# Performance work log

Measured on AMD Instinct MI355X. Metric: run time of the kernel, lower is better.

Reference implementation:

```python
import jax, jax.numpy as jnp
import numpy as np

D_MODEL = 1024
D_FF = 286
NUM_REL = 2
EPS = 1e-6


def setup_inputs() -> dict:
    key = jax.random.key(0)
    ks = jax.random.split(key, 8)
    N, E = 20000, 320000
    hidden_states = jax.random.normal(ks[0], (N, D_MODEL), dtype=jnp.float32)
    edge_index = jax.random.randint(ks[1], (2, E), 0, N, dtype=jnp.int64)
    edge_type = jax.random.randint(ks[2], (E,), 0, NUM_REL, dtype=jnp.int64)
    # learned parameters
    ln_weight = jnp.ones((D_MODEL,), dtype=jnp.float32)
    W_rel = jax.random.normal(ks[3], (NUM_REL, D_MODEL, D_FF), dtype=jnp.float32) * (1.0 / np.sqrt(D_MODEL))
    W_root = jax.random.normal(ks[4], (D_MODEL, D_FF), dtype=jnp.float32) * (1.0 / np.sqrt(D_MODEL))
    conv_bias = jnp.zeros((D_FF,), dtype=jnp.float32)
    wo_weight = jax.random.normal(ks[5], (D_FF, D_MODEL), dtype=jnp.float32) * (1.0 / np.sqrt(D_FF))
    return {"hidden_states": hidden_states, "edge_index": edge_index, "edge_type": edge_type,
            "ln_weight": ln_weight, "W_rel": W_rel, "W_root": W_root,
            "conv_bias": conv_bias, "wo_weight": wo_weight}


def t5_layer_norm(x, weight):
    # T5-style: RMS only, no mean subtraction, no bias; variance in fp32
    var = jnp.mean(jnp.square(x.astype(jnp.float32)), axis=-1, keepdims=True)
    return weight * (x * jax.lax.rsqrt(var + EPS))


def rgcn_conv(x, edge_index, edge_type, W_rel, W_root, bias):
    # PyG RGCNConv with aggr='mean' per relation, root weight, bias.
    N = x.shape[0]
    src, dst = edge_index[0], edge_index[1]
    h_src = x[src]  # [E, d_model] gather
    out = x @ W_root + bias  # root term, [N, d_ff]
    for r in range(NUM_REL):
        w = (edge_type == r).astype(x.dtype)  # [E]
        msg = (h_src @ W_rel[r]) * w[:, None]  # [E, d_ff]
        sums = jax.ops.segment_sum(msg, dst, num_segments=N)  # [N, d_ff]
        cnt = jax.ops.segment_sum(w, dst, num_segments=N)  # [N]
        out = out + sums / jnp.maximum(cnt, 1.0)[:, None]
    return out


def reference(hidden_states, edge_index, edge_type, ln_weight, W_rel, W_root, conv_bias, wo_weight):
    norm_x = t5_layer_norm(hidden_states, ln_weight)
    y = jax.nn.elu(rgcn_conv(norm_x, edge_index, edge_type, W_rel, W_root, conv_bias))
    # dropout layers are identity in eval mode
    y = y @ wo_weight  # [N, d_model], Linear(d_ff, d_model, bias=False)
    return hidden_states + y
```

## Files before the change

kernel.cpp:

```cpp
#include <hip/hip_runtime.h>
#include <hip/hip_bf16.h>


typedef __bf16  bf16x8  __attribute__((ext_vector_type(8)));
typedef float   floatx4 __attribute__((ext_vector_type(4)));

#define NNODE   20000
#define DMODEL  1024
#define DFF     286
#define DFFP    288
#define NDW     144
#define NPAIR   72

typedef __attribute__((address_space(1))) const void* gptr_t;
typedef __attribute__((address_space(3))) void*       lptr_t;

struct alignas(8) bf4 { __bf16 x, y, z, w; };

__device__ __forceinline__ float bflo(unsigned u) {
    union { unsigned u; float f; } c; c.u = u << 16; return c.f;
}
__device__ __forceinline__ float bfhi(unsigned u) {
    union { unsigned u; float f; } c; c.u = u & 0xffff0000u; return c.f;
}
__device__ __forceinline__ unsigned packbf(float a, float b) {
    union { __bf16 h[2]; unsigned u; } c;
    c.h[0] = (__bf16)a; c.h[1] = (__bf16)b; return c.u;
}
__device__ __forceinline__ float elu1(float v) {
    return v > 0.0f ? v : (expf(v) - 1.0f);
}

__global__ __launch_bounds__(256) void k_transpose_cast(
    const float* __restrict__ src, __bf16* __restrict__ dst,
    int K, int N, int Kout, int Nout)
{
    __shared__ float t[32][33];
    int tx = threadIdx.x & 31, ty = threadIdx.x >> 5;
    int k0 = blockIdx.x * 32, n0 = blockIdx.y * 32;
    #pragma unroll
    for (int r = 0; r < 4; ++r) {
        int k = k0 + ty + r * 8, n = n0 + tx;
        t[ty + r * 8][tx] = (k < K && n < N) ? src[(size_t)k * N + n] : 0.0f;
    }
    __syncthreads();
    #pragma unroll
    for (int r = 0; r < 4; ++r) {
        int n = n0 + ty + r * 8, k = k0 + tx;
        if (n < Nout && k < Kout) dst[(size_t)n * Kout + k] = (__bf16)t[tx][ty + r * 8];
    }
}

__global__ __launch_bounds__(256) void k_rmsnorm(
    const float* __restrict__ x, const float* __restrict__ w,
    __bf16* __restrict__ out)
{
    int row = blockIdx.x;
    int t = threadIdx.x;
    float4 v = reinterpret_cast<const float4*>(x + (size_t)row * DMODEL)[t];
    float ss = v.x * v.x + v.y * v.y + v.z * v.z + v.w * v.w;
    #pragma unroll
    for (int off = 32; off; off >>= 1) ss += __shfl_down(ss, off, 64);
    __shared__ float red[4];
    int lane = t & 63, wv = t >> 6;
    if (lane == 0) red[wv] = ss;
    __syncthreads();
    float tot = red[0] + red[1] + red[2] + red[3];
    float scale = rsqrtf(tot * (1.0f / (float)DMODEL) + 1e-6f);
    float4 wv4 = reinterpret_cast<const float4*>(w)[t];
    bf4 o;
    o.x = (__bf16)(v.x * scale * wv4.x);
    o.y = (__bf16)(v.y * scale * wv4.y);
    o.z = (__bf16)(v.z * scale * wv4.z);
    o.w = (__bf16)(v.w * scale * wv4.w);
    reinterpret_cast<bf4*>(out + (size_t)row * DMODEL)[t] = o;
}

__global__ __launch_bounds__(256, 2) void k_gemm1(
    const __bf16* __restrict__ A, const __bf16* __restrict__ Broot,
    const __bf16* __restrict__ Brel, __bf16* __restrict__ P)
{
    const int bid = blockIdx.x;
    const int mt = bid / 3, mz = bid - mt * 3;
    const __bf16* B = (mz == 0) ? Broot : (Brel + (size_t)(mz - 1) * DFFP * DMODEL);
    __bf16* out = P + (size_t)mz * NNODE * DFFP;

    const int m0 = mt * 128;
    const int tid = threadIdx.x;
    const int lane = tid & 63, wave = tid >> 6;
    const int wm = wave >> 1, wn = wave & 1;
    const int quad = lane >> 4, l16 = lane & 15;

    __shared__ __align__(16) __bf16 As[128 * 32];
    __shared__ __align__(16) __bf16 Bs[288 * 32];

    floatx4 zero = {0.f, 0.f, 0.f, 0.f};
    floatx4 acc[4][9];
    #pragma unroll
    for (int i = 0; i < 4; ++i)
        #pragma unroll
        for (int j = 0; j < 9; ++j) acc[i][j] = zero;

    const int crow = lane >> 2;
    const int ccol = (lane & 3) * 8;

    for (int k0 = 0; k0 < DMODEL; k0 += 32) {
        #pragma unroll
        for (int ii = 0; ii < 7; ++ii) {
            int c = wave + ii * 4;
            if (c < 8) {
                int row = c * 16 + crow;
                int grow = m0 + row; if (grow > NNODE - 1) grow = NNODE - 1;
                __builtin_amdgcn_global_load_lds(
                    (gptr_t)(A + (size_t)grow * DMODEL + k0 + ccol),
                    (lptr_t)(As + c * 512), 16, 0, 0);
            } else if (c < 26) {
                int nrow = (c - 8) * 16 + crow;
                __builtin_amdgcn_global_load_lds(
                    (gptr_t)(B + (size_t)nrow * DMODEL + k0 + ccol),
                    (lptr_t)(Bs + (c - 8) * 512), 16, 0, 0);
            }
        }
        __syncthreads();
        bf16x8 af[4], bq[9];
        #pragma unroll
        for (int i = 0; i < 4; ++i)
            af[i] = *reinterpret_cast<const bf16x8*>(As + (wm * 64 + i * 16 + l16) * 32 + quad * 8);
        #pragma unroll
        for (int j = 0; j < 9; ++j)
            bq[j] = *reinterpret_cast<const bf16x8*>(Bs + (wn * 144 + j * 16 + l16) * 32 + quad * 8);
        #pragma unroll
        for (int i = 0; i < 4; ++i)
            #pragma unroll
            for (int j = 0; j < 9; ++j)
                acc[i][j] = __builtin_amdgcn_mfma_f32_16x16x32_bf16(af[i], bq[j], acc[i][j], 0, 0, 0);
        __syncthreads();
    }
    #pragma unroll
    for (int i = 0; i < 4; ++i) {
        int rbase = m0 + wm * 64 + i * 16 + quad * 4;
        #pragma unroll
        for (int j = 0; j < 9; ++j) {
            int col = wn * 144 + j * 16 + l16;
            #pragma unroll
            for (int rr = 0; rr < 4; ++rr) {
                int row = rbase + rr;
                if (row < NNODE) out[(size_t)row * DFFP + col] = (__bf16)acc[i][j][rr];
            }
        }
    }
}

__global__ __launch_bounds__(256) void k_hist(
    const int* __restrict__ ei, int* __restrict__ bcnt, int E)
{
    int t = blockIdx.x * 256 + threadIdx.x;
    if (t < E) atomicAdd(&bcnt[ei[E + t]], 1);
}

__global__ __launch_bounds__(1024) void k_scan(
    const int* __restrict__ bcnt, int* __restrict__ boff, int* __restrict__ bcur)
{
    const int CH = 20;
    __shared__ int s[1024];
    int t = threadIdx.x;
    int base = t * CH;
    int loc[CH];
    int sum = 0;
    #pragma unroll
    for (int i = 0; i < CH; ++i) {
        int idx = base + i;
        int v = (idx < NNODE) ? bcnt[idx] : 0;
        loc[i] = sum; sum += v;
    }
    s[t] = sum;
    __syncthreads();
    for (int off = 1; off < 1024; off <<= 1) {
        int v = (t >= off) ? s[t - off] : 0;
        __syncthreads();
        s[t] += v;
        __syncthreads();
    }
    int prev = (t == 0) ? 0 : s[t - 1];
    #pragma unroll
    for (int i = 0; i < CH; ++i) {
        int idx = base + i;
        if (idx < NNODE) { int o = prev + loc[i]; boff[idx] = o; bcur[idx] = o; }
    }
    if (t == 1023) boff[NNODE] = s[1023];
}

__global__ __launch_bounds__(256) void k_scatter_idx(
    const int* __restrict__ ei, const int* __restrict__ et,
    int* __restrict__ bcur, int* __restrict__ sorted, int E)
{
    int t = blockIdx.x * 256 + threadIdx.x;
    if (t >= E) return;
    int src = ei[t], dst = ei[E + t], r = et[t];
    int pos = atomicAdd(&bcur[dst], 1);
    sorted[pos] = src | (r << 20);
}

__global__ __launch_bounds__(256) void k_reduce(
    const int* __restrict__ boff, const int* __restrict__ sorted,
    const __bf16* __restrict__ proj, const float* __restrict__ bias,
    __bf16* __restrict__ y2)
{
    int b = blockIdx.x * 4 + (threadIdx.x >> 6);
    int lane = threadIdx.x & 63;
    int start = boff[b], end = boff[b + 1];
    bool t8 = lane < 8;

    const uint2* base1 = reinterpret_cast<const uint2*>(proj + (size_t)NNODE * DFFP);
    const size_t relstride = (size_t)NNODE * NPAIR;

    float a0[4] = {0.f, 0.f, 0.f, 0.f}, b0a[4] = {0.f, 0.f, 0.f, 0.f};
    float a1[4] = {0.f, 0.f, 0.f, 0.f}, b1a[4] = {0.f, 0.f, 0.f, 0.f};
    float c0 = 0.f, c1 = 0.f;
    uint2 zz; zz.x = 0u; zz.y = 0u;

    int e = start;
    for (; e + 4 <= end; e += 4) {
        uint2 x[4], y[4]; float w1[4];
        #pragma unroll
        for (int u = 0; u < 4; ++u) {
            int p = sorted[e + u];
            int ri = p >> 20;
            w1[u] = (float)ri;
            const uint2* row = base1 + (size_t)(p & 0xFFFFF) * NPAIR + (ri ? relstride : 0);
            x[u] = row[lane];
            y[u] = t8 ? row[64 + lane] : zz;
        }
        #pragma unroll
        for (int u = 0; u < 4; ++u) {
            float W1 = w1[u], W0 = 1.0f - W1;
            c0 += W0; c1 += W1;
            float v0 = bflo(x[u].x), v1 = bfhi(x[u].x), v2 = bflo(x[u].y), v3 = bfhi(x[u].y);
            a0[0] += W0 * v0; a1[0] += W1 * v0;
            a0[1] += W0 * v1; a1[1] += W1 * v1;
            a0[2] += W0 * v2; a1[2] += W1 * v2;
            a0[3] += W0 * v3; a1[3] += W1 * v3;
            float u0 = bflo(y[u].x), u1 = bfhi(y[u].x), u2 = bflo(y[u].y), u3 = bfhi(y[u].y);
            b0a[0] += W0 * u0; b1a[0] += W1 * u0;
            b0a[1] += W0 * u1; b1a[1] += W1 * u1;
            b0a[2] += W0 * u2; b1a[2] += W1 * u2;
            b0a[3] += W0 * u3; b1a[3] += W1 * u3;
        }
    }
    for (; e < end; ++e) {
        int p = sorted[e];
        int ri = p >> 20;
        float W1 = (float)ri, W0 = 1.0f - W1;
        const uint2* row = base1 + (size_t)(p & 0xFFFFF) * NPAIR + (ri ? relstride : 0);
        uint2 x = row[lane];
        uint2 y = t8 ? row[64 + lane] : zz;
        c0 += W0; c1 += W1;
        float v0 = bflo(x.x), v1 = bfhi(x.x), v2 = bflo(x.y), v3 = bfhi(x.y);
        a0[0] += W0 * v0; a1[0] += W1 * v0;
        a0[1] += W0 * v1; a1[1] += W1 * v1;
        a0[2] += W0 * v2; a1[2] += W1 * v2;
        a0[3] += W0 * v3; a1[3] += W1 * v3;
        float u0 = bflo(y.x), u1 = bfhi(y.x), u2 = bflo(y.y), u3 = bfhi(y.y);
        b0a[0] += W0 * u0; b1a[0] += W1 * u0;
        b0a[1] += W0 * u1; b1a[1] += W1 * u1;
        b0a[2] += W0 * u2; b1a[2] += W1 * u2;
        b0a[3] += W0 * u3; b1a[3] += W1 * u3;
    }

    float inv0 = 1.0f / fmaxf(c0, 1.0f);
    float inv1 = 1.0f / fmaxf(c1, 1.0f);

    const uint2* rootrow = reinterpret_cast<const uint2*>(proj) + (size_t)b * NPAIR;
    uint2* outrow = reinterpret_cast<uint2*>(y2) + (size_t)b * NPAIR;

    {
        uint2 rt = rootrow[lane];
        int f = 4 * lane;
        float v0 = bflo(rt.x) + bias[f]     + a0[0] * inv0 + a1[0] * inv1;
        float v1 = bfhi(rt.x) + bias[f + 1] + a0[1] * inv0 + a1[1] * inv1;
        float v2 = bflo(rt.y) + bias[f + 2] + a0[2] * inv0 + a1[2] * inv1;
        float v3 = bfhi(rt.y) + bias[f + 3] + a0[3] * inv0 + a1[3] * inv1;
        uint2 o; o.x = packbf(elu1(v0), elu1(v1)); o.y = packbf(elu1(v2), elu1(v3));
        outrow[lane] = o;
    }
    if (t8) {
        uint2 rt = rootrow[64 + lane];
        int f = 256 + 4 * lane;
        float g0 = (f     < DFF) ? bias[f]     : 0.0f;
        float g1 = (f + 1 < DFF) ? bias[f + 1] : 0.0f;
        float g2 = (f + 2 < DFF) ? bias[f + 2] : 0.0f;
        float g3 = (f + 3 < DFF) ? bias[f + 3] : 0.0f;
        float v0 = bflo(rt.x) + g0 + b0a[0] * inv0 + b1a[0] * inv1;
        float v1 = bfhi(rt.x) + g1 + b0a[1] * inv0 + b1a[1] * inv1;
        float v2 = bflo(rt.y) + g2 + b0a[2] * inv0 + b1a[2] * inv1;
        float v3 = bfhi(rt.y) + g3 + b0a[3] * inv0 + b1a[3] * inv1;
        uint2 o; o.x = packbf(elu1(v0), elu1(v1)); o.y = packbf(elu1(v2), elu1(v3));
        outrow[64 + lane] = o;
    }
}

__global__ __launch_bounds__(256) void k_gemm2(
    const __bf16* __restrict__ A, const __bf16* __restrict__ Bt,
    const float* __restrict__ hidden, float* __restrict__ out)
{
    const int m0 = blockIdx.x * 128;
    const int n0 = blockIdx.y * 128;
    const int tid = threadIdx.x;
    const int lane = tid & 63, wave = tid >> 6;
    const int wm = wave >> 1, wn = wave & 1;
    const int quad = lane >> 4, l16 = lane & 15;

    __shared__ __align__(16) __bf16 As[2][128 * 32];
    __shared__ __align__(16) __bf16 Bs[2][128 * 32];

    floatx4 zero = {0.f, 0.f, 0.f, 0.f};
    floatx4 acc[4][4];
    #pragma unroll
    for (int i = 0; i < 4; ++i)
        #pragma unroll
        for (int j = 0; j < 4; ++j) acc[i][j] = zero;

    const int crow = lane >> 2, ccol = (lane & 3) * 8;

    auto stage = [&](int kk, int buf) {
        #pragma unroll
        for (int ii = 0; ii < 4; ++ii) {
            int c = wave + ii * 4;
            if (c < 8) {
                int grow = m0 + c * 16 + crow; if (grow > NNODE - 1) grow = NNODE - 1;
                __builtin_amdgcn_global_load_lds(
                    (gptr_t)(A + (size_t)grow * DFFP + kk + ccol),
                    (lptr_t)(As[buf] + c * 512), 16, 0, 0);
            } else {
                int nrow = n0 + (c - 8) * 16 + crow;
                __builtin_amdgcn_global_load_lds(
                    (gptr_t)(Bt + (size_t)nrow * DFFP + kk + ccol),
                    (lptr_t)(Bs[buf] + (c - 8) * 512), 16, 0, 0);
            }
        }
    };

    stage(0, 0);
    __syncthreads();
    for (int ks = 0; ks < 9; ++ks) {
        int buf = ks & 1;
        if (ks < 8) stage((ks + 1) * 32, buf ^ 1);
        bf16x8 af[4], bq[4];
        #pragma unroll
        for (int i = 0; i < 4; ++i)
            af[i] = *reinterpret_cast<const bf16x8*>(As[buf] + (wm * 64 + i * 16 + l16) * 32 + quad * 8);
        #pragma unroll
        for (int j = 0; j < 4; ++j)
            bq[j] = *reinterpret_cast<const bf16x8*>(Bs[buf] + (wn * 64 + j * 16 + l16) * 32 + quad * 8);
        #pragma unroll
        for (int i = 0; i < 4; ++i)
            #pragma unroll
            for (int j = 0; j < 4; ++j)
                acc[i][j] = __builtin_amdgcn_mfma_f32_16x16x32_bf16(af[i], bq[j], acc[i][j], 0, 0, 0);
        __syncthreads();
    }

    {
        float* smbase = reinterpret_cast<float*>(wave < 2 ? (__bf16*)As[0] : (__bf16*)Bs[0]);
        float* smw = smbase + (wave & 1) * 1088;
        const int rsub = lane >> 4;
        const int colf = n0 + wn * 64 + l16 * 4;
        #pragma unroll
        for (int i = 0; i < 4; ++i) {
            #pragma unroll
            for (int j = 0; j < 4; ++j)
                #pragma unroll
                for (int rr = 0; rr < 4; ++rr)
                    smw[(quad * 4 + rr) * 68 + j * 16 + l16] = acc[i][j][rr];
            const int rbase = m0 + wm * 64 + i * 16;
            floatx4 h[4];
            #pragma unroll
            for (int k = 0; k < 4; ++k) {
                int row = rbase + k * 4 + rsub;
                if (row > NNODE - 1) row = NNODE - 1;
                h[k] = __builtin_nontemporal_load(
                    reinterpret_cast<const floatx4*>(hidden + (size_t)row * DMODEL + colf));
            }
            #pragma unroll
            for (int k = 0; k < 4; ++k) {
                int row = rbase + k * 4 + rsub;
                floatx4 v = *reinterpret_cast<const floatx4*>(
                    smw + (k * 4 + rsub) * 68 + l16 * 4);
                if (row < NNODE)
                    __builtin_nontemporal_store(h[k] + v,
                        reinterpret_cast<floatx4*>(out + (size_t)row * DMODEL + colf));
            }
        }
    }
}

extern "C" void kernel_launch(void* const* d_in, const int* in_sizes, int n_in,
                              void* d_out, int out_size, void* d_ws, size_t ws_size,
                              hipStream_t stream)
{
    const float* hidden   = (const float*)d_in[0];
    const int*   ei       = (const int*)  d_in[1];
    const int*   et       = (const int*)  d_in[2];
    const float* ln_w     = (const float*)d_in[3];
    const float* W_rel    = (const float*)d_in[4];
    const float* W_root   = (const float*)d_in[5];
    const float* bias     = (const float*)d_in[6];
    const float* wo       = (const float*)d_in[7];
    float* out = (float*)d_out;

    const int E = in_sizes[1] / 2;

    char* ws = (char*)d_ws;
    __bf16* norm_bf = (__bf16*)(ws + 0);
    __bf16* proj    = (__bf16*)(ws + 40960000);
    __bf16* y2      = (__bf16*)(ws + 75520000);
    __bf16* wroot_t = (__bf16*)(ws + 87040000);
    __bf16* wrel_t  = (__bf16*)(ws + 87629824);
    __bf16* wo_t    = (__bf16*)(ws + 88809472);
    int*    bcnt    = (int*)   (ws + 89399296);
    int*    boff    = (int*)   (ws + 89479296);
    int*    bcur    = (int*)   (ws + 89559312);
    int*    sorted  = (int*)   (ws + 89639312);

    hipMemsetAsync(bcnt, 0, 80000, stream);

    {
        dim3 g1((DMODEL + 31) / 32, (DFFP + 31) / 32);
        k_transpose_cast<<<g1, 256, 0, stream>>>(W_root, wroot_t, DMODEL, DFF, DMODEL, DFFP);
        k_transpose_cast<<<g1, 256, 0, stream>>>(W_rel, wrel_t, DMODEL, DFF, DMODEL, DFFP);
        k_transpose_cast<<<g1, 256, 0, stream>>>(W_rel + (size_t)DMODEL * DFF,
                                                 wrel_t + (size_t)DFFP * DMODEL,
                                                 DMODEL, DFF, DMODEL, DFFP);
        dim3 g2((DFFP + 31) / 32, (DMODEL + 31) / 32);
        k_transpose_cast<<<g2, 256, 0, stream>>>(wo, wo_t, DFF, DMODEL, DFFP, DMODEL);
    }

    k_rmsnorm<<<NNODE, 256, 0, stream>>>(hidden, ln_w, norm_bf);

    k_hist<<<(E + 255) / 256, 256, 0, stream>>>(ei, bcnt, E);
    k_scan<<<1, 1024, 0, stream>>>(bcnt, boff, bcur);
    k_scatter_idx<<<(E + 255) / 256, 256, 0, stream>>>(ei, et, bcur, sorted, E);

    {
        int nmt = (NNODE + 127) / 128;
        k_gemm1<<<nmt * 3, 256, 0, stream>>>(norm_bf, wroot_t, wrel_t, proj);
    }

    k_reduce<<<NNODE / 4, 256, 0, stream>>>(boff, sorted, proj, bias, y2);

    {
        dim3 grid((NNODE + 127) / 128, DMODEL / 128);
        k_gemm2<<<grid, 256, 0, stream>>>(y2, wo_t, hidden, out);
    }
}
```

Baseline: 356.0 us.

## Double-buffer GEMM1 LDS, swizzle LDS tiles, and remap blocks across XCDs

The first GEMM now double-buffers its A and B LDS tiles so the global-to-LDS load of the next K slice overlaps the MFMA work on the current one. Both GEMMs also XOR-swizzle the 16-byte column chunk on store and load to reduce LDS bank conflicts. Block IDs in GEMM1 are remapped so consecutive tiles land on the same XCD, which is meant to improve L2 reuse of the shared B operand. Doubling GEMM1's LDS use may lower occupancy below the requested two blocks per CU.

```diff
diff --git a/kernel.cpp b/kernel.cpp
--- a/kernel.cpp
+++ b/kernel.cpp
@@ -80,7 +80,11 @@
     const __bf16* __restrict__ A, const __bf16* __restrict__ Broot,
     const __bf16* __restrict__ Brel, __bf16* __restrict__ P)
 {
-    const int bid = blockIdx.x;
+    const int nwg = gridDim.x;
+    const int q = nwg >> 3, r = nwg & 7;
+    const int xcd = blockIdx.x & 7, sub = blockIdx.x >> 3;
+    const int bid = (xcd < r ? xcd * (q + 1) : r * (q + 1) + (xcd - r) * q) + sub;
+
     const int mt = bid / 3, mz = bid - mt * 3;
     const __bf16* B = (mz == 0) ? Broot : (Brel + (size_t)(mz - 1) * DFFP * DMODEL);
     __bf16* out = P + (size_t)mz * NNODE * DFFP;
@@ -91,8 +95,8 @@
     const int wm = wave >> 1, wn = wave & 1;
     const int quad = lane >> 4, l16 = lane & 15;
 
-    __shared__ __align__(16) __bf16 As[128 * 32];
-    __shared__ __align__(16) __bf16 Bs[288 * 32];
+    __shared__ __align__(16) __bf16 As[2][128 * 32];
+    __shared__ __align__(16) __bf16 Bs[2][288 * 32];
 
     floatx4 zero = {0.f, 0.f, 0.f, 0.f};
     floatx4 acc[4][9];
@@ -102,9 +106,10 @@
         for (int j = 0; j < 9; ++j) acc[i][j] = zero;
 
     const int crow = lane >> 2;
-    const int ccol = (lane & 3) * 8;
-
-    for (int k0 = 0; k0 < DMODEL; k0 += 32) {
+    const int ccol = ((lane & 3) ^ ((lane >> 3) & 3)) * 8;
+    const int sq   = (quad ^ ((l16 >> 1) & 3)) * 8;
+
+    auto stage = [&](int k0, int buf) {
         #pragma unroll
         for (int ii = 0; ii < 7; ++ii) {
             int c = wave + ii * 4;
@@ -113,22 +118,28 @@
                 int grow = m0 + row; if (grow > NNODE - 1) grow = NNODE - 1;
                 __builtin_amdgcn_global_load_lds(
                     (gptr_t)(A + (size_t)grow * DMODEL + k0 + ccol),
-                    (lptr_t)(As + c * 512), 16, 0, 0);
+                    (lptr_t)(As[buf] + c * 512), 16, 0, 0);
             } else if (c < 26) {
                 int nrow = (c - 8) * 16 + crow;
                 __builtin_amdgcn_global_load_lds(
                     (gptr_t)(B + (size_t)nrow * DMODEL + k0 + ccol),
-                    (lptr_t)(Bs + (c - 8) * 512), 16, 0, 0);
+                    (lptr_t)(Bs[buf] + (c - 8) * 512), 16, 0, 0);
             }
         }
-        __syncthreads();
+    };
+
+    stage(0, 0);
+    __syncthreads();
+    for (int ks = 0; ks < 32; ++ks) {
+        int buf = ks & 1;
+        if (ks < 31) stage((ks + 1) * 32, buf ^ 1);
         bf16x8 af[4], bq[9];
         #pragma unroll
         for (int i = 0; i < 4; ++i)
-            af[i] = *reinterpret_cast<const bf16x8*>(As + (wm * 64 + i * 16 + l16) * 32 + quad * 8);
+            af[i] = *reinterpret_cast<const bf16x8*>(As[buf] + (wm * 64 + i * 16 + l16) * 32 + sq);
         #pragma unroll
         for (int j = 0; j < 9; ++j)
-            bq[j] = *reinterpret_cast<const bf16x8*>(Bs + (wn * 144 + j * 16 + l16) * 32 + quad * 8);
+            bq[j] = *reinterpret_cast<const bf16x8*>(Bs[buf] + (wn * 144 + j * 16 + l16) * 32 + sq);
         #pragma unroll
         for (int i = 0; i < 4; ++i)
             #pragma unroll
@@ -320,7 +331,9 @@
         #pragma unroll
         for (int j = 0; j < 4; ++j) acc[i][j] = zero;
 
-    const int crow = lane >> 2, ccol = (lane & 3) * 8;
+    const int crow = lane >> 2;
+    const int ccol = ((lane & 3) ^ ((lane >> 3) & 3)) * 8;
+    const int sq   = (quad ^ ((l16 >> 1) & 3)) * 8;
 
     auto stage = [&](int kk, int buf) {
         #pragma unroll
@@ -348,10 +361,10 @@
         bf16x8 af[4], bq[4];
         #pragma unroll
         for (int i = 0; i < 4; ++i)
-            af[i] = *reinterpret_cast<const bf16x8*>(As[buf] + (wm * 64 + i * 16 + l16) * 32 + quad * 8);
+            af[i] = *reinterpret_cast<const bf16x8*>(As[buf] + (wm * 64 + i * 16 + l16) * 32 + sq);
         #pragma unroll
         for (int j = 0; j < 4; ++j)
-            bq[j] = *reinterpret_cast<const bf16x8*>(Bs[buf] + (wn * 64 + j * 16 + l16) * 32 + quad * 8);
+            bq[j] = *reinterpret_cast<const bf16x8*>(Bs[buf] + (wn * 64 + j * 16 + l16) * 32 + sq);
         #pragma unroll
         for (int i = 0; i < 4; ++i)
             #pragma unroll
```

New measurement: 350.3 us. Within noise of the previous version (-1.6%).
